# Kernel tuning notes

Hardware: AMD Instinct MI355X
Metric: run time of the kernel (lower is better)

Reference implementation:

```python
import jax, jax.numpy as jnp
import numpy as np

BETA = 0.25
TEMP = 1.0
K = 1024          # codebook_size
DIM = 256         # dim == z_dim


def setup_inputs() -> dict:
    key = jax.random.key(0)
    k1, k2, k3 = jax.random.split(key, 3)
    x = jax.random.normal(k1, (8, 4096, DIM), dtype=jnp.float32)
    # Linear: kaiming_uniform -> sqrt(3/fan_in) * U(-1,1); bias init_bias=0 -> zeros
    W = np.sqrt(3.0 / DIM) * (jax.random.uniform(k2, (DIM, DIM), dtype=jnp.float32) * 2 - 1)
    b = jnp.zeros((DIM,), dtype=jnp.float32)
    # embedding: uniform(-1/K, 1/K)
    emb = jax.random.uniform(k3, (K, DIM), dtype=jnp.float32,
                             minval=-1.0 / K, maxval=1.0 / K)
    return {"x": x, "W": W, "b": b, "emb": emb}


def reference(x, W, b, emb):
    # proj_in: x @ W.T + b
    z = jnp.einsum('bld,od->blo', x, W) + b                     # [B, L, D]
    # squared-L2 distances to codebook (use_norm=False branch)
    dist = (jnp.sum(z * z, axis=-1, keepdims=True)
            + jnp.sum(emb * emb, axis=1)
            - 2.0 * jnp.einsum('bld,nd->bln', z, emb))           # [B, L, K]
    indices = jnp.argmin(dist, axis=-1)                          # [B, L] int
    # ste_prob computed in torch forward (affects grads via one_hot, not outputs)
    quant = emb[indices]                                         # [B, L, D]
    # commitment + codebook loss (training=True)
    loss = (BETA * jnp.mean((jax.lax.stop_gradient(quant) - z) ** 2)
            + jnp.mean((quant - jax.lax.stop_gradient(z)) ** 2))
    # straight-through estimator
    quant = z + jax.lax.stop_gradient(quant - z)
    return quant, indices, loss
```

## Files before the change

kernel.cpp:

```cpp
#include <hip/hip_runtime.h>
#include <hip/hip_bf16.h>

#define TT 32768
#define DD 256
#define KK 1024
#define B_S 5e-4f

typedef __attribute__((ext_vector_type(8)))  short bf16x8;
typedef __attribute__((ext_vector_type(4)))  short bf16x4s;
typedef __attribute__((ext_vector_type(16))) float f32x16;

static inline __device__ short f2bf(float v) {
    __hip_bfloat16 h = __float2bfloat16(v);
    return __builtin_bit_cast(short, h);
}
static inline __device__ float bf2f(short s) {
    __hip_bfloat16 h = __builtin_bit_cast(__hip_bfloat16, s);
    return __bfloat162float(h);
}

static inline __device__ void gload16(const void* g, void* l) {
    __builtin_amdgcn_global_load_lds(
        (const __attribute__((address_space(1))) void*)g,
        (__attribute__((address_space(3))) void*)l,
        16, 0, 0);
}

__global__ void k_ee(const float* __restrict__ emb, float* __restrict__ ee,
                     int* __restrict__ g_nf) {
    if (blockIdx.x == 0 && threadIdx.x == 0) g_nf[0] = 0;
    int n = blockIdx.x * 256 + threadIdx.x;
    if (n >= KK) return;
    const float4* r = (const float4*)(emb + (size_t)n * DD);
    float s = 0.f;
#pragma unroll
    for (int i = 0; i < DD / 4; ++i) {
        float4 v = r[i];
        s += v.x * v.x + v.y * v.y + v.z * v.z + v.w * v.w;
    }
    ee[n] = s;
}

__global__ void k_pack(const float* __restrict__ emb, short* __restrict__ pemb,
                       float4* __restrict__ embP4) {
    int u = blockIdx.x * 256 + threadIdx.x;
    int lane = u & 63;
    int ks  = (u >> 6) & 1, nb = (u >> 7) & 3;
    int kbi = (u >> 9) & 7, nc = (u >> 12) & 7;
    int n = nc * 128 + nb * 32 + (lane & 31);
    int k = kbi * 32 + ks * 16 + (lane >> 5) * 8;
    const float* src = emb + (size_t)n * DD + k;
    float4 v0 = *(const float4*)(src);
    float4 v1 = *(const float4*)(src + 4);
    bf16x8 hb = { f2bf(v0.x), f2bf(v0.y), f2bf(v0.z), f2bf(v0.w),
                  f2bf(v1.x), f2bf(v1.y), f2bf(v1.z), f2bf(v1.w) };
    *(bf16x8*)(pemb + (size_t)u * 8) = hb;
    embP4[(size_t)(k >> 2) * KK + n]       = v0;
    embP4[(size_t)((k >> 2) + 1) * KK + n] = v1;
}

__global__ void k_wpack(const float* __restrict__ W, short* __restrict__ Wp) {
    int idx = blockIdx.x * 256 + threadIdx.x;
    int lane = idx & 63;
    int ks = (idx >> 6) & 1, cb = (idx >> 7) & 3;
    int g  = (idx >> 9) & 1, kb = (idx >> 10) & 7;
    int row = g * 128 + cb * 32 + (lane & 31);
    int col = kb * 32 + ks * 16 + (lane >> 5) * 8;
    const float* src = W + (size_t)row * DD + col;
    float4 v0 = *(const float4*)(src);
    float4 v1 = *(const float4*)(src + 4);
    float e[8] = {v0.x, v0.y, v0.z, v0.w, v1.x, v1.y, v1.z, v1.w};
    bf16x8 s1, s2, s3;
#pragma unroll
    for (int q = 0; q < 8; ++q) {
        short h1 = f2bf(e[q]); float r1 = e[q] - bf2f(h1);
        short h2 = f2bf(r1);   float r2 = r1 - bf2f(h2);
        short h3 = f2bf(r2);
        s1[q] = h1; s2[q] = h2; s3[q] = h3;
    }
    size_t c0 = ((((size_t)kb * 3 + 0) * 2 + g) * 4 + cb) * 2 + ks;
    size_t c1 = ((((size_t)kb * 3 + 1) * 2 + g) * 4 + cb) * 2 + ks;
    size_t c2 = ((((size_t)kb * 3 + 2) * 2 + g) * 4 + cb) * 2 + ks;
    *(bf16x8*)(Wp + c0 * 512 + lane * 8) = s1;
    *(bf16x8*)(Wp + c1 * 512 + lane * 8) = s2;
    *(bf16x8*)(Wp + c2 * 512 + lane * 8) = s3;
}

#define PW 40

__launch_bounds__(256, 1)
__global__ void k_proj(const float* __restrict__ x, const short* __restrict__ Wp,
                       const float* __restrict__ bias, float* __restrict__ z) {
    __shared__ __align__(16) short Ax[3][64 * PW];
    const int tid = threadIdx.x;
    const int w = tid >> 6, lane = tid & 63;
    const int l31 = lane & 31, h = lane >> 5;
    const int t0 = blockIdx.x * 64;
    const int wt = (w & 1) * 32;
    const int g  = (w >> 1);

    f32x16 acc[4];
#pragma unroll
    for (int cb = 0; cb < 4; ++cb)
#pragma unroll
        for (int r = 0; r < 16; ++r) acc[cb][r] = 0.f;

    for (int kb8 = 0; kb8 < 8; ++kb8) {
        __syncthreads();
        bf16x8 wb[2][4][3];
#pragma unroll
        for (int ks = 0; ks < 2; ++ks)
#pragma unroll
            for (int cb = 0; cb < 4; ++cb)
#pragma unroll
                for (int s = 0; s < 3; ++s) {
                    size_t c = ((((size_t)kb8 * 3 + s) * 2 + g) * 4 + cb) * 2 + ks;
                    wb[ks][cb][s] = *(const bf16x8*)(Wp + c * 512 + lane * 8);
                }
#pragma unroll
        for (int j = 0; j < 2; ++j) {
            int idx = j * 256 + tid, row = idx >> 3, c4 = idx & 7;
            float4 v = *(const float4*)(x + (size_t)(t0 + row) * DD + kb8 * 32 + c4 * 4);
            float e[4] = {v.x, v.y, v.z, v.w};
            bf16x4s s1, s2, s3;
#pragma unroll
            for (int q = 0; q < 4; ++q) {
                short h1 = f2bf(e[q]); float r1 = e[q] - bf2f(h1);
                short h2 = f2bf(r1);   float r2 = r1 - bf2f(h2);
                short h3 = f2bf(r2);
                s1[q] = h1; s2[q] = h2; s3[q] = h3;
            }
            int a = row * PW + c4 * 4;
            *(bf16x4s*)&Ax[0][a] = s1; *(bf16x4s*)&Ax[1][a] = s2; *(bf16x4s*)&Ax[2][a] = s3;
        }
        __syncthreads();
#pragma unroll
        for (int ks = 0; ks < 2; ++ks) {
            int ao = (wt + l31) * PW + ks * 16 + h * 8;
            bf16x8 a1 = *(bf16x8*)&Ax[0][ao];
            bf16x8 a2 = *(bf16x8*)&Ax[1][ao];
            bf16x8 a3 = *(bf16x8*)&Ax[2][ao];
#pragma unroll
            for (int cb = 0; cb < 4; ++cb) {
                bf16x8 b1 = wb[ks][cb][0];
                bf16x8 b2 = wb[ks][cb][1];
                bf16x8 b3 = wb[ks][cb][2];
                acc[cb] = __builtin_amdgcn_mfma_f32_32x32x16_bf16(a1, b3, acc[cb], 0, 0, 0);
                acc[cb] = __builtin_amdgcn_mfma_f32_32x32x16_bf16(a2, b2, acc[cb], 0, 0, 0);
                acc[cb] = __builtin_amdgcn_mfma_f32_32x32x16_bf16(a3, b1, acc[cb], 0, 0, 0);
                acc[cb] = __builtin_amdgcn_mfma_f32_32x32x16_bf16(a1, b2, acc[cb], 0, 0, 0);
                acc[cb] = __builtin_amdgcn_mfma_f32_32x32x16_bf16(a2, b1, acc[cb], 0, 0, 0);
                acc[cb] = __builtin_amdgcn_mfma_f32_32x32x16_bf16(a1, b1, acc[cb], 0, 0, 0);
            }
        }
    }
#pragma unroll
    for (int cb = 0; cb < 4; ++cb) {
        int col = g * 128 + cb * 32 + l31;
        float bc = bias[col];
#pragma unroll
        for (int r = 0; r < 16; ++r) {
            int row = (r & 3) + 8 * (r >> 2) + 4 * h;
            z[(size_t)(t0 + wt + row) * DD + col] = acc[cb][r] + bc;
        }
    }
}

#define SW 264

__launch_bounds__(256, 1)
__global__ void k_screen(const float* __restrict__ z, const short* __restrict__ pemb,
                         const float* __restrict__ ee_g, float* __restrict__ out_idx) {
    __shared__ __align__(16) char smem[65536];
    __shared__ float ee_s[1024];
    __shared__ float zzs[64];

    short* A_s   = (short*)smem;
    float* zpart = (float*)(smem + 33792);
    const int tid = threadIdx.x;
    const int w = tid >> 6, lane = tid & 63;
    const int l31 = lane & 31, h = lane >> 5;
    const int t0 = blockIdx.x * 64;
    const int wr = (w >> 1) * 32;
    const int hw = w & 1;

#pragma unroll
    for (int i = 0; i < 4; ++i) ee_s[i * 256 + tid] = ee_g[i * 256 + tid];

#pragma unroll
    for (int i = 0; i < 16; ++i) {
        int tl = i * 4 + w;
        float4 v = *(const float4*)(z + (size_t)(t0 + tl) * DD + lane * 4);
        float sq = v.x * v.x + v.y * v.y + v.z * v.z + v.w * v.w;
        zpart[tl * 65 + lane] = sq;
        bf16x4s hb = {f2bf(v.x), f2bf(v.y), f2bf(v.z), f2bf(v.w)};
        *(bf16x4s*)&A_s[tl * SW + lane * 4] = hb;
    }
    __syncthreads();

    if (tid < 64) {
        float t_[32];
#pragma unroll
        for (int l = 0; l < 32; ++l) t_[l] = zpart[tid * 65 + l] + zpart[tid * 65 + l + 32];
#pragma unroll
        for (int l = 0; l < 16; ++l) t_[l] = t_[l] + t_[l + 16];
#pragma unroll
        for (int l = 0; l < 8; ++l)  t_[l] = t_[l] + t_[l + 8];
#pragma unroll
        for (int l = 0; l < 4; ++l)  t_[l] = t_[l] + t_[l + 4];
#pragma unroll
        for (int l = 0; l < 2; ++l)  t_[l] = t_[l] + t_[l + 2];
        zzs[tid] = t_[0] + t_[1];
    }

    bf16x8 af[16];
#pragma unroll
    for (int kbi = 0; kbi < 8; ++kbi)
#pragma unroll
        for (int ks = 0; ks < 2; ++ks)
            af[kbi * 2 + ks] = *(bf16x8*)&A_s[(wr + l31) * SW + kbi * 32 + ks * 16 + h * 8];
    __syncthreads();

    float zf[16];
#pragma unroll
    for (int r = 0; r < 16; ++r) zf[r] = zzs[wr + (r & 3) + 8 * (r >> 2) + 4 * h];

    const char* pB = (const char*)pemb;
#pragma unroll
    for (int j = 0; j < 8; ++j)
        gload16(pB + j * 8192 + w * 1024 + lane * 16, smem + j * 4096 + w * 1024);

    float bestv[16], secv[16]; int besti[16];
#pragma unroll
    for (int r = 0; r < 16; ++r) { bestv[r] = 1e30f; secv[r] = 1e30f; besti[r] = 0; }

    for (int ph = 0; ph < 16; ++ph) {
        const int buf = ph & 1;
        char* Bb = smem + buf * 32768;
        asm volatile("s_waitcnt vmcnt(0)" ::: "memory");
        __syncthreads();
        if (ph < 15) {
            const int nn = ph + 1;
            const char* src = pB + (size_t)(nn >> 1) * 65536 + (nn & 1) * 4096;
            char* dst = smem + (buf ^ 1) * 32768;
#pragma unroll
            for (int j = 0; j < 8; ++j)
                gload16(src + j * 8192 + w * 1024 + lane * 16, dst + j * 4096 + w * 1024);
        }
        __builtin_amdgcn_sched_barrier(0);
        f32x16 accA, accB;
#pragma unroll
        for (int r = 0; r < 16; ++r) { accA[r] = 0.f; accB[r] = 0.f; }
        __builtin_amdgcn_s_setprio(1);
#pragma unroll
        for (int kbi = 0; kbi < 4; ++kbi) {
            bf16x8 a0b = *(bf16x8*)(Bb + kbi * 4096 + (hw * 2 + 0) * 1024 + lane * 16);
            bf16x8 a1b = *(bf16x8*)(Bb + kbi * 4096 + (hw * 2 + 1) * 1024 + lane * 16);
            bf16x8 b0b = *(bf16x8*)(Bb + (kbi + 4) * 4096 + (hw * 2 + 0) * 1024 + lane * 16);
            bf16x8 b1b = *(bf16x8*)(Bb + (kbi + 4) * 4096 + (hw * 2 + 1) * 1024 + lane * 16);
            accA = __builtin_amdgcn_mfma_f32_32x32x16_bf16(af[kbi * 2 + 0], a0b, accA, 0, 0, 0);
            accB = __builtin_amdgcn_mfma_f32_32x32x16_bf16(af[(kbi + 4) * 2 + 0], b0b, accB, 0, 0, 0);
            accA = __builtin_amdgcn_mfma_f32_32x32x16_bf16(af[kbi * 2 + 1], a1b, accA, 0, 0, 0);
            accB = __builtin_amdgcn_mfma_f32_32x32x16_bf16(af[(kbi + 4) * 2 + 1], b1b, accB, 0, 0, 0);
        }
        __builtin_amdgcn_s_setprio(0);
        {
            int n = (ph >> 1) * 128 + (ph & 1) * 64 + hw * 32 + l31;
            float en = ee_s[n];
#pragma unroll
            for (int r = 0; r < 16; ++r) {
                float u = zf[r] + en;
                float d = accA[r] + accB[r];
                float sc = fmaf(-2.f, d, u);
                if (sc < bestv[r])      { secv[r] = bestv[r]; bestv[r] = sc; besti[r] = n; }
                else if (sc < secv[r])  { secv[r] = sc; }
            }
        }
    }

    __syncthreads();
    float* entV = (float*)smem;
    float* entS = entV + 4224;
    int*   entI = (int*)(entV + 8448);
    const int slot = hw * 32 + l31;
#pragma unroll
    for (int r = 0; r < 16; ++r) {
        int tr = wr + (r & 3) + 8 * (r >> 2) + 4 * h;
        entV[tr * 66 + slot] = bestv[r];
        entS[tr * 66 + slot] = secv[r];
        entI[tr * 66 + slot] = besti[r];
    }
    __syncthreads();
    if (tid < 64) {
        float bv = entV[tid * 66 + 0];
        float sv = entS[tid * 66 + 0];
        int   bi = entI[tid * 66 + 0];
        for (int e = 1; e < 64; ++e) {
            float v  = entV[tid * 66 + e];
            float s2 = entS[tid * 66 + e];
            int   i  = entI[tid * 66 + e];
            float mx = fmaxf(bv, v);
            sv = fminf(fminf(sv, s2), mx);
            if (v < bv || (v == bv && i < bi)) { bv = v; bi = i; }
        }
        float flag = ((sv - bv) < B_S) ? 4096.0f : 0.0f;
        out_idx[t0 + tid] = (float)bi + flag;
    }
}

__global__ void k_compact(const float* __restrict__ out_idx, int* __restrict__ g_nf,
                          int* __restrict__ g_list) {
    __shared__ int wbase[4];
    __shared__ int bbase;
    const int tid = threadIdx.x;
    const int t = blockIdx.x * 256 + tid;
    const int wid = tid >> 6, lane = tid & 63;
    bool fl = out_idx[t] >= 4096.0f;
    unsigned long long m = __ballot(fl);
    if (lane == 0) wbase[wid] = __popcll(m);
    __syncthreads();
    if (tid == 0) {
        int s = 0;
#pragma unroll
        for (int i = 0; i < 4; ++i) { int c = wbase[i]; wbase[i] = s; s += c; }
        bbase = atomicAdd(g_nf, s);
    }
    __syncthreads();
    if (fl) {
        int rank = __popcll(m & ((1ull << lane) - 1ull));
        g_list[bbase + wbase[wid] + rank] = t;
    }
}

#define RB 8

__launch_bounds__(256, 2)
__global__ void k_rescoreT(const float* __restrict__ z, const float4* __restrict__ embP4,
                           const float* __restrict__ ee_g, const int* __restrict__ g_nf,
                           const int* __restrict__ g_list, float* __restrict__ out_idx) {
    __shared__ float zrows[RB][256];
    __shared__ float zz8[RB];
    __shared__ int   toks[RB];
    __shared__ float rv_s[RB][4]; __shared__ int ri_s[RB][4];
    const int tid = threadIdx.x;
    const int w = tid >> 6, lane = tid & 63;
    const int nf = g_nf[0];

    for (int base = blockIdx.x * RB; base < nf; base += gridDim.x * RB) {
        __syncthreads();
        if (tid < RB) toks[tid] = (base + tid < nf) ? g_list[base + tid] : -1;
        __syncthreads();
#pragma unroll
        for (int qq = 0; qq < RB; ++qq) {
            int tok = toks[qq];
            zrows[qq][tid] = (tok >= 0) ? z[(size_t)tok * DD + tid] : 0.f;
        }
        __syncthreads();
        for (int qq = w; qq < RB; qq += 4) {
            float s = 0.f;
#pragma unroll
            for (int k = 0; k < 4; ++k) { float vv = zrows[qq][lane + 64 * k]; s += vv * vv; }
#pragma unroll
            for (int o = 32; o; o >>= 1) s += __shfl_xor(s, o);
            if (lane == 0) zz8[qq] = s;
        }
        __syncthreads();

        float en4[4];
#pragma unroll
        for (int p = 0; p < 4; ++p) en4[p] = ee_g[p * 256 + tid];

        float d[4][RB];
#pragma unroll
        for (int p = 0; p < 4; ++p)
#pragma unroll
            for (int q = 0; q < RB; ++q) d[p][q] = 0.f;

        float4 eA[4], eB[4], zA[RB], zB[RB];
#pragma unroll
        for (int p = 0; p < 4; ++p) eA[p] = embP4[(size_t)0 * KK + p * 256 + tid];
#pragma unroll
        for (int q = 0; q < RB; ++q) zA[q] = *(const float4*)&zrows[q][0];

        for (int k4 = 0; k4 < 64; k4 += 2) {
#pragma unroll
            for (int p = 0; p < 4; ++p) eB[p] = embP4[(size_t)(k4 + 1) * KK + p * 256 + tid];
#pragma unroll
            for (int q = 0; q < RB; ++q) zB[q] = *(const float4*)&zrows[q][(k4 + 1) * 4];
#pragma unroll
            for (int p = 0; p < 4; ++p)
#pragma unroll
                for (int q = 0; q < RB; ++q) {
                    d[p][q] = fmaf(eA[p].x, zA[q].x, d[p][q]);
                    d[p][q] = fmaf(eA[p].y, zA[q].y, d[p][q]);
                    d[p][q] = fmaf(eA[p].z, zA[q].z, d[p][q]);
                    d[p][q] = fmaf(eA[p].w, zA[q].w, d[p][q]);
                }
            if (k4 < 62) {
#pragma unroll
                for (int p = 0; p < 4; ++p) eA[p] = embP4[(size_t)(k4 + 2) * KK + p * 256 + tid];
#pragma unroll
                for (int q = 0; q < RB; ++q) zA[q] = *(const float4*)&zrows[q][(k4 + 2) * 4];
            }
#pragma unroll
            for (int p = 0; p < 4; ++p)
#pragma unroll
                for (int q = 0; q < RB; ++q) {
                    d[p][q] = fmaf(eB[p].x, zB[q].x, d[p][q]);
                    d[p][q] = fmaf(eB[p].y, zB[q].y, d[p][q]);
                    d[p][q] = fmaf(eB[p].z, zB[q].z, d[p][q]);
                    d[p][q] = fmaf(eB[p].w, zB[q].w, d[p][q]);
                }
        }

        float bv[RB]; int bi[RB];
#pragma unroll
        for (int q = 0; q < RB; ++q) { bv[q] = 1e30f; bi[q] = 0; }
#pragma unroll
        for (int p = 0; p < 4; ++p) {
            const int n = p * 256 + tid;
#pragma unroll
            for (int q = 0; q < RB; ++q) {
                float u = zz8[q] + en4[p];
                float s = fmaf(-2.f, d[p][q], u);
                if (s < bv[q]) { bv[q] = s; bi[q] = n; }
            }
        }
        for (int q = 0; q < RB; ++q) {
            float v = bv[q]; int i = bi[q];
#pragma unroll
            for (int o = 1; o < 64; o <<= 1) {
                float ov = __shfl_xor(v, o); int oi = __shfl_xor(i, o);
                if (ov < v || (ov == v && oi < i)) { v = ov; i = oi; }
            }
            if (lane == 0) { rv_s[q][w] = v; ri_s[q][w] = i; }
        }
        __syncthreads();
        if (tid < RB) {
            int tk = toks[tid];
            if (tk >= 0) {
                float fv = rv_s[tid][0]; int fi = ri_s[tid][0];
#pragma unroll
                for (int ww = 1; ww < 4; ++ww) {
                    if (rv_s[tid][ww] < fv || (rv_s[tid][ww] == fv && ri_s[tid][ww] < fi)) {
                        fv = rv_s[tid][ww]; fi = ri_s[tid][ww];
                    }
                }
                out_idx[tk] = (float)fi;
            }
        }
    }
}

__global__ void k_gather(float* __restrict__ zq, const float* __restrict__ emb,
                         const float* __restrict__ out_idx, float* __restrict__ partial) {
    __shared__ float red[4];
    const int tid = threadIdx.x;
    const int t0 = blockIdx.x * 128;
    const int tl = tid >> 1, part = tid & 1;
    int widx = (int)out_idx[t0 + tl];
    widx = min(max(widx, 0), KK - 1);
    const float* erow = emb + (size_t)widx * DD;
    float* qrow = zq + (size_t)(t0 + tl) * DD;
    float lsum = 0.f;
#pragma unroll
    for (int k = 0; k < 32; ++k) {
        int f = part + 2 * k;
        float4 e  = *(const float4*)(erow + f * 4);
        float4 zv = *(const float4*)(qrow + f * 4);
        float dx = e.x - zv.x, dy = e.y - zv.y, dz = e.z - zv.z, dw = e.w - zv.w;
        lsum += dx * dx + dy * dy + dz * dz + dw * dw;
        *(float4*)(qrow + f * 4) = e;
    }
#pragma unroll
    for (int off = 32; off; off >>= 1) lsum += __shfl_down(lsum, off);
    if ((tid & 63) == 0) red[tid >> 6] = lsum;
    __syncthreads();
    if (tid == 0) partial[blockIdx.x] = red[0] + red[1] + red[2] + red[3];
}

__global__ void k_loss(const float* __restrict__ partial, float* __restrict__ out_loss) {
    __shared__ float red[4];
    int tid = threadIdx.x;
    float s = partial[tid];
#pragma unroll
    for (int off = 32; off; off >>= 1) s += __shfl_down(s, off);
    if ((tid & 63) == 0) red[tid >> 6] = s;
    __syncthreads();
    if (tid == 0)
        out_loss[0] = (red[0] + red[1] + red[2] + red[3]) * (1.25f / 8388608.0f);
}

extern "C" void kernel_launch(void* const* d_in, const int* in_sizes, int n_in,
                              void* d_out, int out_size, void* d_ws, size_t ws_size,
                              hipStream_t stream) {
    const float* x   = (const float*)d_in[0];
    const float* W   = (const float*)d_in[1];
    const float* b   = (const float*)d_in[2];
    const float* emb = (const float*)d_in[3];

    float* out   = (float*)d_out;
    float* quant = out;
    float* oidx  = out + (size_t)TT * DD;
    float* oloss = oidx + TT;

    float* wsf     = (float*)d_ws;
    float* ee      = wsf;
    float* partial = wsf + 1024;
    short* pemb    = (short*)(wsf + 1280);
    int*   g_nf    = (int*)(wsf + 132352);
    int*   g_list  = (int*)(wsf + 132353);
    float4* embP4  = (float4*)(wsf + 165124);
    short* Wp      = (short*)(wsf + 427268);

    k_ee      <<<KK / 256, 256, 0, stream>>>(emb, ee, g_nf);
    k_pack    <<<128,      256, 0, stream>>>(emb, pemb, embP4);
    k_wpack   <<<32,       256, 0, stream>>>(W, Wp);
    k_proj    <<<TT / 64,  256, 0, stream>>>(x, Wp, b, quant);
    k_screen  <<<TT / 64,  256, 0, stream>>>(quant, pemb, ee, oidx);
    k_compact <<<TT / 256, 256, 0, stream>>>(oidx, g_nf, g_list);
    k_rescoreT<<<512,      256, 0, stream>>>(quant, embP4, ee, g_nf, g_list, oidx);
    k_gather  <<<TT / 128, 256, 0, stream>>>(quant, emb, oidx, partial);
    k_loss    <<<1,        256, 0, stream>>>(partial, oloss);
}
```

Before: 264.7 us.

## Halve token tiles in proj and screen, stream codebook from global into registers

Both k_proj and k_screen now process 32 tokens per block instead of 64, with twice as many blocks and higher launch-bound occupancy. In k_screen the LDS double-buffered global_load_lds staging of the packed codebook is replaced by direct register prefetch from global. Each wave owns a 32-code slice and reduces its best and second-best candidates with warp shuffles before a small cross-wave merge. This aims to raise occupancy and cut LDS traffic and barriers. In exchange each block re-reads the whole codebook from global/L2 for only half as many tokens, so L2 traffic doubles.

New measurement: 568.3 us. +114.6%, slower.

```diff
diff --git a/kernel.cpp b/kernel.cpp
--- a/kernel.cpp
+++ b/kernel.cpp
@@ -17,13 +17,6 @@
 static inline __device__ float bf2f(short s) {
     __hip_bfloat16 h = __builtin_bit_cast(__hip_bfloat16, s);
     return __bfloat162float(h);
-}
-
-static inline __device__ void gload16(const void* g, void* l) {
-    __builtin_amdgcn_global_load_lds(
-        (const __attribute__((address_space(1))) void*)g,
-        (__attribute__((address_space(3))) void*)l,
-        16, 0, 0);
 }
 
 __global__ void k_ee(const float* __restrict__ emb, float* __restrict__ ee,
@@ -88,38 +81,36 @@
 
 #define PW 40
 
-__launch_bounds__(256, 1)
+__launch_bounds__(256, 2)
 __global__ void k_proj(const float* __restrict__ x, const short* __restrict__ Wp,
                        const float* __restrict__ bias, float* __restrict__ z) {
-    __shared__ __align__(16) short Ax[3][64 * PW];
+    __shared__ __align__(16) short Ax[3][32 * PW];
     const int tid = threadIdx.x;
     const int w = tid >> 6, lane = tid & 63;
     const int l31 = lane & 31, h = lane >> 5;
-    const int t0 = blockIdx.x * 64;
-    const int wt = (w & 1) * 32;
-    const int g  = (w >> 1);
-
-    f32x16 acc[4];
-#pragma unroll
-    for (int cb = 0; cb < 4; ++cb)
+    const int t0 = blockIdx.x * 32;
+
+    f32x16 acc[2];
+#pragma unroll
+    for (int cb = 0; cb < 2; ++cb)
 #pragma unroll
         for (int r = 0; r < 16; ++r) acc[cb][r] = 0.f;
 
     for (int kb8 = 0; kb8 < 8; ++kb8) {
         __syncthreads();
-        bf16x8 wb[2][4][3];
+        bf16x8 wb[2][2][3];
 #pragma unroll
         for (int ks = 0; ks < 2; ++ks)
 #pragma unroll
-            for (int cb = 0; cb < 4; ++cb)
+            for (int cb = 0; cb < 2; ++cb)
 #pragma unroll
                 for (int s = 0; s < 3; ++s) {
-                    size_t c = ((((size_t)kb8 * 3 + s) * 2 + g) * 4 + cb) * 2 + ks;
+                    size_t c = ((((size_t)kb8 * 3 + s) * 2 + (w >> 1)) * 4
+                                + ((w & 1) * 2 + cb)) * 2 + ks;
                     wb[ks][cb][s] = *(const bf16x8*)(Wp + c * 512 + lane * 8);
                 }
-#pragma unroll
-        for (int j = 0; j < 2; ++j) {
-            int idx = j * 256 + tid, row = idx >> 3, c4 = idx & 7;
+        {
+            int row = tid >> 3, c4 = tid & 7;
             float4 v = *(const float4*)(x + (size_t)(t0 + row) * DD + kb8 * 32 + c4 * 4);
             float e[4] = {v.x, v.y, v.z, v.w};
             bf16x4s s1, s2, s3;
@@ -136,12 +127,12 @@
         __syncthreads();
 #pragma unroll
         for (int ks = 0; ks < 2; ++ks) {
-            int ao = (wt + l31) * PW + ks * 16 + h * 8;
+            int ao = l31 * PW + ks * 16 + h * 8;
             bf16x8 a1 = *(bf16x8*)&Ax[0][ao];
             bf16x8 a2 = *(bf16x8*)&Ax[1][ao];
             bf16x8 a3 = *(bf16x8*)&Ax[2][ao];
 #pragma unroll
-            for (int cb = 0; cb < 4; ++cb) {
+            for (int cb = 0; cb < 2; ++cb) {
                 bf16x8 b1 = wb[ks][cb][0];
                 bf16x8 b2 = wb[ks][cb][1];
                 bf16x8 b3 = wb[ks][cb][2];
@@ -155,150 +146,132 @@
         }
     }
 #pragma unroll
-    for (int cb = 0; cb < 4; ++cb) {
-        int col = g * 128 + cb * 32 + l31;
+    for (int cb = 0; cb < 2; ++cb) {
+        int col = w * 64 + cb * 32 + l31;
         float bc = bias[col];
 #pragma unroll
         for (int r = 0; r < 16; ++r) {
             int row = (r & 3) + 8 * (r >> 2) + 4 * h;
-            z[(size_t)(t0 + wt + row) * DD + col] = acc[cb][r] + bc;
+            z[(size_t)(t0 + row) * DD + col] = acc[cb][r] + bc;
         }
     }
 }
 
 #define SW 264
 
-__launch_bounds__(256, 1)
+__launch_bounds__(256, 3)
 __global__ void k_screen(const float* __restrict__ z, const short* __restrict__ pemb,
                          const float* __restrict__ ee_g, float* __restrict__ out_idx) {
-    __shared__ __align__(16) char smem[65536];
+    __shared__ __align__(16) short A_s[32 * SW];
     __shared__ float ee_s[1024];
-    __shared__ float zzs[64];
-
-    short* A_s   = (short*)smem;
-    float* zpart = (float*)(smem + 33792);
+    __shared__ float zzs[32];
+    __shared__ float r_bv[32][5]; __shared__ int r_bi[32][5]; __shared__ float r_sv[32][5];
+
     const int tid = threadIdx.x;
     const int w = tid >> 6, lane = tid & 63;
     const int l31 = lane & 31, h = lane >> 5;
-    const int t0 = blockIdx.x * 64;
-    const int wr = (w >> 1) * 32;
-    const int hw = w & 1;
+    const int t0 = blockIdx.x * 32;
 
 #pragma unroll
     for (int i = 0; i < 4; ++i) ee_s[i * 256 + tid] = ee_g[i * 256 + tid];
 
 #pragma unroll
-    for (int i = 0; i < 16; ++i) {
+    for (int i = 0; i < 8; ++i) {
         int tl = i * 4 + w;
         float4 v = *(const float4*)(z + (size_t)(t0 + tl) * DD + lane * 4);
         float sq = v.x * v.x + v.y * v.y + v.z * v.z + v.w * v.w;
-        zpart[tl * 65 + lane] = sq;
+#pragma unroll
+        for (int o = 32; o; o >>= 1) sq += __shfl_xor(sq, o);
+        if (lane == 0) zzs[tl] = sq;
         bf16x4s hb = {f2bf(v.x), f2bf(v.y), f2bf(v.z), f2bf(v.w)};
         *(bf16x4s*)&A_s[tl * SW + lane * 4] = hb;
     }
     __syncthreads();
 
-    if (tid < 64) {
-        float t_[32];
-#pragma unroll
-        for (int l = 0; l < 32; ++l) t_[l] = zpart[tid * 65 + l] + zpart[tid * 65 + l + 32];
-#pragma unroll
-        for (int l = 0; l < 16; ++l) t_[l] = t_[l] + t_[l + 16];
-#pragma unroll
-        for (int l = 0; l < 8; ++l)  t_[l] = t_[l] + t_[l + 8];
-#pragma unroll
-        for (int l = 0; l < 4; ++l)  t_[l] = t_[l] + t_[l + 4];
-#pragma unroll
-        for (int l = 0; l < 2; ++l)  t_[l] = t_[l] + t_[l + 2];
-        zzs[tid] = t_[0] + t_[1];
-    }
-
-    bf16x8 af[16];
-#pragma unroll
-    for (int kbi = 0; kbi < 8; ++kbi)
-#pragma unroll
-        for (int ks = 0; ks < 2; ++ks)
-            af[kbi * 2 + ks] = *(bf16x8*)&A_s[(wr + l31) * SW + kbi * 32 + ks * 16 + h * 8];
-    __syncthreads();
-
-    float zf[16];
-#pragma unroll
-    for (int r = 0; r < 16; ++r) zf[r] = zzs[wr + (r & 3) + 8 * (r >> 2) + 4 * h];
-
-    const char* pB = (const char*)pemb;
-#pragma unroll
-    for (int j = 0; j < 8; ++j)
-        gload16(pB + j * 8192 + w * 1024 + lane * 16, smem + j * 4096 + w * 1024);
+    const int u0 = ((w * 2 + 0) * 64 + lane) * 8;
+    const int u1 = ((w * 2 + 1) * 64 + lane) * 8;
+
+    bf16x8 B0A = *(const bf16x8*)(pemb + u0);
+    bf16x8 B1A = *(const bf16x8*)(pemb + u1);
+    bf16x8 B0B, B1B;
 
     float bestv[16], secv[16]; int besti[16];
 #pragma unroll
     for (int r = 0; r < 16; ++r) { bestv[r] = 1e30f; secv[r] = 1e30f; besti[r] = 0; }
 
-    for (int ph = 0; ph < 16; ++ph) {
-        const int buf = ph & 1;
-        char* Bb = smem + buf * 32768;
-        asm volatile("s_waitcnt vmcnt(0)" ::: "memory");
-        __syncthreads();
-        if (ph < 15) {
-            const int nn = ph + 1;
-            const char* src = pB + (size_t)(nn >> 1) * 65536 + (nn & 1) * 4096;
-            char* dst = smem + (buf ^ 1) * 32768;
-#pragma unroll
-            for (int j = 0; j < 8; ++j)
-                gload16(src + j * 8192 + w * 1024 + lane * 16, dst + j * 4096 + w * 1024);
-        }
-        __builtin_amdgcn_sched_barrier(0);
-        f32x16 accA, accB;
-#pragma unroll
-        for (int r = 0; r < 16; ++r) { accA[r] = 0.f; accB[r] = 0.f; }
-        __builtin_amdgcn_s_setprio(1);
-#pragma unroll
-        for (int kbi = 0; kbi < 4; ++kbi) {
-            bf16x8 a0b = *(bf16x8*)(Bb + kbi * 4096 + (hw * 2 + 0) * 1024 + lane * 16);
-            bf16x8 a1b = *(bf16x8*)(Bb + kbi * 4096 + (hw * 2 + 1) * 1024 + lane * 16);
-            bf16x8 b0b = *(bf16x8*)(Bb + (kbi + 4) * 4096 + (hw * 2 + 0) * 1024 + lane * 16);
-            bf16x8 b1b = *(bf16x8*)(Bb + (kbi + 4) * 4096 + (hw * 2 + 1) * 1024 + lane * 16);
-            accA = __builtin_amdgcn_mfma_f32_32x32x16_bf16(af[kbi * 2 + 0], a0b, accA, 0, 0, 0);
-            accB = __builtin_amdgcn_mfma_f32_32x32x16_bf16(af[(kbi + 4) * 2 + 0], b0b, accB, 0, 0, 0);
-            accA = __builtin_amdgcn_mfma_f32_32x32x16_bf16(af[kbi * 2 + 1], a1b, accA, 0, 0, 0);
-            accB = __builtin_amdgcn_mfma_f32_32x32x16_bf16(af[(kbi + 4) * 2 + 1], b1b, accB, 0, 0, 0);
-        }
-        __builtin_amdgcn_s_setprio(0);
+    f32x16 acc;
+    for (int t = 0; t < 64; t += 2) {
         {
-            int n = (ph >> 1) * 128 + (ph & 1) * 64 + hw * 32 + l31;
-            float en = ee_s[n];
-#pragma unroll
-            for (int r = 0; r < 16; ++r) {
-                float u = zf[r] + en;
-                float d = accA[r] + accB[r];
-                float sc = fmaf(-2.f, d, u);
-                if (sc < bestv[r])      { secv[r] = bestv[r]; bestv[r] = sc; besti[r] = n; }
-                else if (sc < secv[r])  { secv[r] = sc; }
-            }
-        }
-    }
-
-    __syncthreads();
-    float* entV = (float*)smem;
-    float* entS = entV + 4224;
-    int*   entI = (int*)(entV + 8448);
-    const int slot = hw * 32 + l31;
-#pragma unroll
-    for (int r = 0; r < 16; ++r) {
-        int tr = wr + (r & 3) + 8 * (r >> 2) + 4 * h;
-        entV[tr * 66 + slot] = bestv[r];
-        entS[tr * 66 + slot] = secv[r];
-        entI[tr * 66 + slot] = besti[r];
-    }
-    __syncthreads();
-    if (tid < 64) {
-        float bv = entV[tid * 66 + 0];
-        float sv = entS[tid * 66 + 0];
-        int   bi = entI[tid * 66 + 0];
-        for (int e = 1; e < 64; ++e) {
-            float v  = entV[tid * 66 + e];
-            float s2 = entS[tid * 66 + e];
-            int   i  = entI[tid * 66 + e];
+            const short* gt = pemb + (size_t)(t + 1) * 4096;
+            B0B = *(const bf16x8*)(gt + u0);
+            B1B = *(const bf16x8*)(gt + u1);
+        }
+        {
+            const int kbi = t & 7;
+            if (kbi == 0) {
+#pragma unroll
+                for (int r = 0; r < 16; ++r) acc[r] = 0.f;
+            }
+            bf16x8 a0 = *(bf16x8*)&A_s[l31 * SW + kbi * 32 + 0 * 16 + h * 8];
+            bf16x8 a1 = *(bf16x8*)&A_s[l31 * SW + kbi * 32 + 1 * 16 + h * 8];
+            acc = __builtin_amdgcn_mfma_f32_32x32x16_bf16(a0, B0A, acc, 0, 0, 0);
+            acc = __builtin_amdgcn_mfma_f32_32x32x16_bf16(a1, B1A, acc, 0, 0, 0);
+        }
+        if (t < 62) {
+            const short* gt = pemb + (size_t)(t + 2) * 4096;
+            B0A = *(const bf16x8*)(gt + u0);
+            B1A = *(const bf16x8*)(gt + u1);
+        }
+        {
+            const int kbi = (t + 1) & 7;
+            bf16x8 a0 = *(bf16x8*)&A_s[l31 * SW + kbi * 32 + 0 * 16 + h * 8];
+            bf16x8 a1 = *(bf16x8*)&A_s[l31 * SW + kbi * 32 + 1 * 16 + h * 8];
+            acc = __builtin_amdgcn_mfma_f32_32x32x16_bf16(a0, B0B, acc, 0, 0, 0);
+            acc = __builtin_amdgcn_mfma_f32_32x32x16_bf16(a1, B1B, acc, 0, 0, 0);
+            if (kbi == 7) {
+                const int nc = (t + 1) >> 3;
+                const int n = nc * 128 + w * 32 + l31;
+                float en = ee_s[n];
+#pragma unroll
+                for (int r = 0; r < 16; ++r) {
+                    int row = (r & 3) + 8 * (r >> 2) + 4 * h;
+                    float u = zzs[row] + en;
+                    float sc = fmaf(-2.f, acc[r], u);
+                    if (sc < bestv[r])      { secv[r] = bestv[r]; bestv[r] = sc; besti[r] = n; }
+                    else if (sc < secv[r])  { secv[r] = sc; }
+                }
+            }
+        }
+    }
+
+#pragma unroll
+    for (int o = 1; o < 32; o <<= 1) {
+#pragma unroll
+        for (int r = 0; r < 16; ++r) {
+            float ov = __shfl_xor(bestv[r], o);
+            int   oi = __shfl_xor(besti[r], o);
+            float os = __shfl_xor(secv[r], o);
+            float mx = fmaxf(bestv[r], ov);
+            secv[r] = fminf(fminf(secv[r], os), mx);
+            if (ov < bestv[r] || (ov == bestv[r] && oi < besti[r])) { bestv[r] = ov; besti[r] = oi; }
+        }
+    }
+    if (l31 == 0) {
+#pragma unroll
+        for (int r = 0; r < 16; ++r) {
+            int tr = (r & 3) + 8 * (r >> 2) + 4 * h;
+            r_bv[tr][w] = bestv[r]; r_bi[tr][w] = besti[r]; r_sv[tr][w] = secv[r];
+        }
+    }
+    __syncthreads();
+    if (tid < 32) {
+        float bv = r_bv[tid][0], sv = r_sv[tid][0];
+        int   bi = r_bi[tid][0];
+#pragma unroll
+        for (int ww = 1; ww < 4; ++ww) {
+            float v  = r_bv[tid][ww];
+            float s2 = r_sv[tid][ww];
+            int   i  = r_bi[tid][ww];
             float mx = fmaxf(bv, v);
             sv = fminf(fminf(sv, s2), mx);
             if (v < bv || (v == bv && i < bi)) { bv = v; bi = i; }
@@ -516,8 +489,8 @@
     k_ee      <<<KK / 256, 256, 0, stream>>>(emb, ee, g_nf);
     k_pack    <<<128,      256, 0, stream>>>(emb, pemb, embP4);
     k_wpack   <<<32,       256, 0, stream>>>(W, Wp);
-    k_proj    <<<TT / 64,  256, 0, stream>>>(x, Wp, b, quant);
-    k_screen  <<<TT / 64,  256, 0, stream>>>(quant, pemb, ee, oidx);
+    k_proj    <<<TT / 32,  256, 0, stream>>>(x, Wp, b, quant);
+    k_screen  <<<TT / 32,  256, 0, stream>>>(quant, pemb, ee, oidx);
     k_compact <<<TT / 256, 256, 0, stream>>>(oidx, g_nf, g_list);
     k_rescoreT<<<512,      256, 0, stream>>>(quant, embP4, ee, g_nf, g_list, oidx);
     k_gather  <<<TT / 128, 256, 0, stream>>>(quant, emb, oidx, partial);
```
